# Kernel optimization log

Hardware: AMD Instinct MI355X
Metric: run time of the kernel (lower is better)

The kernel has to match this reference:

```python
import jax, jax.numpy as jnp
import numpy as np

INPUT_DIM = 24
HIDDEN = 128
NUM_LAYERS = 3
OUTPUT_DIM = 1


def _lstm_layer(x, Wih, Whh, bih, bhh):
    """Single LSTM layer, PyTorch gate order (i, f, g, o). x: [B,T,D] -> [B,T,H]."""
    B = x.shape[0]
    H = Whh.shape[1]
    # Precompute input projections for all timesteps at once: [B,T,4H]
    xg = jnp.einsum('btd,gd->btg', x, Wih) + bih
    xg = jnp.swapaxes(xg, 0, 1)  # [T,B,4H]
    h0 = jnp.zeros((B, H), x.dtype)
    c0 = jnp.zeros((B, H), x.dtype)

    def step(carry, xt):
        h, c = carry
        gates = xt + h @ Whh.T + bhh  # [B,4H]
        i, f, g, o = jnp.split(gates, 4, axis=-1)
        i = jax.nn.sigmoid(i)
        f = jax.nn.sigmoid(f)
        g = jnp.tanh(g)
        o = jax.nn.sigmoid(o)
        c = f * c + i * g
        h = o * jnp.tanh(c)
        return (h, c), h

    _, hs = jax.lax.scan(step, (h0, c0), xg)  # hs: [T,B,H]
    return jnp.swapaxes(hs, 0, 1)  # [B,T,H]


def setup_inputs() -> dict:
    key = jax.random.key(0)
    ks = jax.random.split(key, 16)
    B, T = 2048, 256
    s = 0.05
    inp = {
        'x': jax.random.normal(ks[0], (B, T, INPUT_DIM), dtype=jnp.float32),
    }
    dims_in = [INPUT_DIM, HIDDEN, HIDDEN]
    for l in range(NUM_LAYERS):
        inp[f'Wih{l}'] = jax.random.normal(ks[1 + 4 * l], (4 * HIDDEN, dims_in[l]), dtype=jnp.float32) * s
        inp[f'Whh{l}'] = jax.random.normal(ks[2 + 4 * l], (4 * HIDDEN, HIDDEN), dtype=jnp.float32) * s
        inp[f'bih{l}'] = jax.random.normal(ks[3 + 4 * l], (4 * HIDDEN,), dtype=jnp.float32) * s
        inp[f'bhh{l}'] = jax.random.normal(ks[4 + 4 * l], (4 * HIDDEN,), dtype=jnp.float32) * s
    inp['Wfc'] = jax.random.normal(ks[13], (OUTPUT_DIM, HIDDEN), dtype=jnp.float32) * s
    inp['bfc'] = jax.random.normal(ks[14], (OUTPUT_DIM,), dtype=jnp.float32) * s
    return inp


def reference(x, Wih0, Whh0, bih0, bhh0, Wih1, Whh1, bih1, bhh1,
              Wih2, Whh2, bih2, bhh2, Wfc, bfc):
    # 3 stacked LSTM layers (dropout inactive in eval mode), zero initial state.
    h = _lstm_layer(x, Wih0, Whh0, bih0, bhh0)
    h = _lstm_layer(h, Wih1, Whh1, bih1, bhh1)
    h = _lstm_layer(h, Wih2, Whh2, bih2, bhh2)
    # Linear projection of the final timestep: [B,1]
    return h[:, -1, :] @ Wfc.T + bfc
```

## Files before the change

### kernel.cpp

```cpp
#include <hip/hip_runtime.h>

#define T_STEPS 256
#define BATCH   2048
#define HID     128
#define ROWS    8

typedef short short8  __attribute__((ext_vector_type(8)));
typedef short short4v __attribute__((ext_vector_type(4)));
typedef float float4v __attribute__((ext_vector_type(4)));

template<bool B> struct BoolC { static constexpr bool value = B; };

__device__ __forceinline__ unsigned short f2bf(float f) {
    unsigned int u = __builtin_bit_cast(unsigned int, f);
    u += 0x7fffu + ((u >> 16) & 1u);
    return (unsigned short)(u >> 16);
}
__device__ __forceinline__ float bf2f(unsigned short b) {
    unsigned int u = ((unsigned int)b) << 16;
    return __builtin_bit_cast(float, u);
}

#if __has_builtin(__builtin_amdgcn_exp2f)
#define EXP2F(x) __builtin_amdgcn_exp2f(x)
#else
#define EXP2F(x) exp2f(x)
#endif
__device__ __forceinline__ float sigf(float x) {
    return __builtin_amdgcn_rcpf(1.0f + EXP2F(x * -1.442695041f));
}
__device__ __forceinline__ float tanh_fast(float x) {
    return 2.0f * __builtin_amdgcn_rcpf(1.0f + EXP2F(x * -2.885390082f)) - 1.0f;
}

__device__ __forceinline__ void block_sync_lds() {
    asm volatile("s_waitcnt lgkmcnt(0)" ::: "memory");
    __builtin_amdgcn_s_barrier();
    __builtin_amdgcn_sched_barrier(0);
}

__device__ __forceinline__ int lposH(int row, int off) {
    return row * 256 + (off ^ ((row & 7) << 4));
}
__device__ __forceinline__ int lposX(int row, int off) {
    return row * 256 + (off ^ ((row & 7) << 4));
}
__device__ __forceinline__ int lposX0(int row, int off) {
    return row * 64 + (off ^ ((row & 3) << 4));
}

__device__ __forceinline__ short8 load_w8(const float* __restrict__ p) {
    float4v a = *reinterpret_cast<const float4v*>(p);
    float4v b = *reinterpret_cast<const float4v*>(p + 4);
    short8 r;
    r[0] = (short)f2bf(a[0]); r[1] = (short)f2bf(a[1]);
    r[2] = (short)f2bf(a[2]); r[3] = (short)f2bf(a[3]);
    r[4] = (short)f2bf(b[0]); r[5] = (short)f2bf(b[1]);
    r[6] = (short)f2bf(b[2]); r[7] = (short)f2bf(b[3]);
    return r;
}

template<bool IS_L0, bool WRITE_H, bool FINAL>
__global__ __launch_bounds__(512, 2)
void lstm_layer(const float* __restrict__ x0,
                const float* __restrict__ Wih,
                const float* __restrict__ Whh,
                const float* __restrict__ bih,
                const float* __restrict__ bhh,
                unsigned short* __restrict__ hbuf,
                const float* __restrict__ Wfc,
                const float* __restrict__ bfc,
                float* __restrict__ out)
{
    constexpr int XKS = IS_L0 ? 1 : 4;
    constexpr int XRB = IS_L0 ? 64 : 256;
    constexpr int HB  = ROWS * 256;
    constexpr int XB  = 16 * XRB;
    constexpr int LDS_TOT = 2 * HB + 2 * XB;
    __shared__ __attribute__((aligned(16))) unsigned char a_lds[LDS_TOT];
    const int XS0 = 2 * HB, XS1 = 2 * HB + XB;

    const int tid  = threadIdx.x;
    const int lane = tid & 63;
    const int wv   = tid >> 6;
    const int b0   = blockIdx.x * ROWS;

    const int t16   = lane & 15;
    const int kgrp8 = (lane >> 4) * 8;
    const int jcol  = 16 * wv + t16;
    const int row0  = ((lane >> 4) & 1) * 4 + ((lane >> 5) & 1) * 2;

    const int g2   = t16 >> 2;
    const int hrow = ((g2 & 1) << 2) | ((g2 >> 1) << 1) | (t16 & 1);
    int aoffH[4];
    #pragma unroll
    for (int ks = 0; ks < 4; ++ks)
        aoffH[ks] = lposH(hrow, ks * 64 + kgrp8 * 2);
    int aoffX[XKS];
    #pragma unroll
    for (int s = 0; s < XKS; ++s)
        aoffX[s] = IS_L0 ? lposX0(t16, kgrp8 * 2)
                         : lposX(t16, s * 64 + kgrp8 * 2);

    const int hwoff0 = lposH(row0,     2 * jcol);
    const int hwoff1 = lposH(row0 + 1, 2 * jcol);

    const int srow4 = tid >> 6, scol4 = tid & 63;
    const int hroff4 = lposH(srow4, scol4 * 4);
    const size_t sgoff4 = (size_t)(b0 + srow4) * HID + scol4 * 2;

    const int sar = tid >> 5, sc8 = tid & 31;
    const int sb  = (sar & 1) | (((sar >> 3) & 1) << 1) | (((sar >> 2) & 1) << 2);
    const int ss  = (sar >> 1) & 1;
    const int xwoff = lposX(sar, sc8 * 8);
    const size_t xgrow = (size_t)(b0 + sb) * HID + sc8 * 4;
    const bool xvalid = tid < 384;
    const int ar0 = xvalid ? tid / 24 : 0, xc = xvalid ? tid % 24 : 0;
    const int xb_ = (ar0 & 1) | (((ar0 >> 3) & 1) << 1) | (((ar0 >> 2) & 1) << 2);
    const int xs  = (ar0 >> 1) & 1;
    const int xw0off = lposX0(ar0, xc * 2);
    const size_t x0row = (size_t)(b0 + xb_) * (T_STEPS * 24) + xc;

    short8 wfh[4][4], wfx[4][XKS];
    float  bias[4];
    #pragma unroll
    for (int q = 0; q < 4; ++q) {
        const int n = 128 * q + jcol;
        bias[q] = bih[n] + bhh[n];
        #pragma unroll
        for (int ks = 0; ks < 4; ++ks)
            wfh[q][ks] = load_w8(Whh + n * 128 + ks * 32 + kgrp8);
        if (IS_L0) {
            if (kgrp8 < 24) wfx[q][0] = load_w8(Wih + n * 24 + kgrp8);
            else            { short8 z = {0,0,0,0,0,0,0,0}; wfx[q][0] = z; }
        } else {
            #pragma unroll
            for (int s = 0; s < 4; ++s)
                wfx[q][s] = load_w8(Wih + n * 128 + s * 32 + kgrp8);
        }
    }

    {
        short8 z = {0,0,0,0,0,0,0,0};
        for (int i = tid * 16; i < LDS_TOT; i += 512 * 16)
            *reinterpret_cast<short8*>(&a_lds[i]) = z;
    }
    __syncthreads();

    short4v xpre = {0, 0, 0, 0};
    float   xpref = 0.f;
    if (!IS_L0) {
        short4v v = *reinterpret_cast<const short4v*>(
            &hbuf[(size_t)(0 + ss) * (BATCH * HID) + xgrow]);
        *reinterpret_cast<short4v*>(&a_lds[XS0 + xwoff]) = v;
        xpre = *reinterpret_cast<const short4v*>(
            &hbuf[(size_t)(2 + ss) * (BATCH * HID) + xgrow]);
    } else if (xvalid) {
        float v = x0[x0row + (size_t)(0 + xs) * 24];
        *reinterpret_cast<unsigned short*>(&a_lds[XS0 + xw0off]) = f2bf(v);
        xpref = x0[x0row + (size_t)(2 + xs) * 24];
    }
    __syncthreads();

    float4v xacc[4];
    #pragma unroll
    for (int q = 0; q < 4; ++q)
        xacc[q] = float4v{bias[q], bias[q], bias[q], bias[q]};
    {
        short8 xa[XKS];
        #pragma unroll
        for (int s = 0; s < XKS; ++s)
            xa[s] = *reinterpret_cast<const short8*>(&a_lds[XS0 + aoffX[s]]);
        #pragma unroll
        for (int s = 0; s < XKS; ++s)
            #pragma unroll
            for (int q = 0; q < 4; ++q)
                xacc[q] = __builtin_amdgcn_mfma_f32_16x16x32_bf16(xa[s], wfx[q][s], xacc[q], 0, 0, 0);
    }

    float creg[2] = {0.f, 0.f};

    auto do_step = [&](int t, auto ODDC) {
        constexpr bool ODD = decltype(ODDC)::value;
        const int rb = ODD ? HB : 0;
        const int wb = ODD ? 0 : HB;
        if (WRITE_H && t > 0) {
            unsigned int hv = *reinterpret_cast<const unsigned int*>(&a_lds[rb + hroff4]);
            *reinterpret_cast<unsigned int*>(
                &hbuf[(size_t)(t - 1) * (BATCH * HID) + sgoff4]) = hv;
        }
        if constexpr (!ODD) {
            const int xsb = ((((t >> 1) & 1) ^ 1) ? XS1 : XS0);
            if (!IS_L0) {
                if (t + 2 + ss < T_STEPS)
                    *reinterpret_cast<short4v*>(&a_lds[xsb + xwoff]) = xpre;
            } else if (xvalid && (t + 2 + xs < T_STEPS))
                *reinterpret_cast<unsigned short*>(&a_lds[xsb + xw0off]) = f2bf(xpref);
        } else {
            if (!IS_L0) {
                if (t + 3 + ss < T_STEPS)
                    xpre = *reinterpret_cast<const short4v*>(
                        &hbuf[(size_t)(t + 3 + ss) * (BATCH * HID) + xgrow]);
            } else if (xvalid && (t + 3 + xs < T_STEPS))
                xpref = x0[x0row + (size_t)(t + 3 + xs) * 24];
        }
        float4v acc[4];
        #pragma unroll
        for (int q = 0; q < 4; ++q) {
            const float a = ODD ? xacc[q][2] : xacc[q][0];
            const float b = ODD ? xacc[q][3] : xacc[q][1];
            acc[q] = float4v{a, b, a, b};
        }
        short8 hva[4];
        #pragma unroll
        for (int ks = 0; ks < 4; ++ks)
            hva[ks] = *reinterpret_cast<const short8*>(&a_lds[rb + aoffH[ks]]);
        __builtin_amdgcn_s_setprio(1);
        #pragma unroll
        for (int ks = 0; ks < 4; ++ks)
            #pragma unroll
            for (int q = 0; q < 4; ++q)
                acc[q] = __builtin_amdgcn_mfma_f32_16x16x32_bf16(hva[ks], wfh[q][ks], acc[q], 0, 0, 0);
        if constexpr (ODD) {
            if (t + 1 < T_STEPS) {
                const int xrb_ = ((((t + 1) >> 1) & 1) ? XS1 : XS0);
                #pragma unroll
                for (int q = 0; q < 4; ++q)
                    xacc[q] = float4v{bias[q], bias[q], bias[q], bias[q]};
                short8 xa[XKS];
                #pragma unroll
                for (int s = 0; s < XKS; ++s)
                    xa[s] = *reinterpret_cast<const short8*>(&a_lds[xrb_ + aoffX[s]]);
                #pragma unroll
                for (int s = 0; s < XKS; ++s)
                    #pragma unroll
                    for (int q = 0; q < 4; ++q)
                        xacc[q] = __builtin_amdgcn_mfma_f32_16x16x32_bf16(xa[s], wfx[q][s], xacc[q], 0, 0, 0);
            }
        }
        __builtin_amdgcn_s_setprio(0);
        const float c0 = sigf(acc[1][0]) * creg[0] + sigf(acc[0][0]) * tanh_fast(acc[2][0]);
        const float c1 = sigf(acc[1][1]) * creg[1] + sigf(acc[0][1]) * tanh_fast(acc[2][1]);
        creg[0] = c0;  creg[1] = c1;
        const float h0 = sigf(acc[3][0]) * tanh_fast(c0);
        const float h1 = sigf(acc[3][1]) * tanh_fast(c1);
        unsigned int packed;
        asm("v_cvt_pk_bf16_f32 %0, %1, %2" : "=v"(packed) : "v"(h0), "v"(h1));
        *reinterpret_cast<unsigned short*>(&a_lds[wb + hwoff0]) =
            (unsigned short)(packed & 0xffffu);
        *reinterpret_cast<unsigned short*>(&a_lds[wb + hwoff1]) =
            (unsigned short)(packed >> 16);
        block_sync_lds();
    };

    for (int th = 0; th < T_STEPS / 2; ++th) {
        do_step(2 * th,     BoolC<false>{});
        do_step(2 * th + 1, BoolC<true>{});
    }
    if (WRITE_H) {
        unsigned int hv = *reinterpret_cast<const unsigned int*>(&a_lds[hroff4]);
        *reinterpret_cast<unsigned int*>(
            &hbuf[(size_t)(T_STEPS - 1) * (BATCH * HID) + sgoff4]) = hv;
    }
    if (FINAL && tid < 128) {
        const int r = tid >> 4, seg = tid & 15;
        float s = 0.f;
        #pragma unroll
        for (int k = 0; k < 8; ++k) {
            const int j = seg * 8 + k;
            s += bf2f(*reinterpret_cast<const unsigned short*>(&a_lds[lposH(r, 2 * j)]))
                 * Wfc[j];
        }
        #pragma unroll
        for (int off = 8; off >= 1; off >>= 1) s += __shfl_xor(s, off);
        if (seg == 0) out[b0 + r] = s + bfc[0];
    }
}

extern "C" void kernel_launch(void* const* d_in, const int* in_sizes, int n_in,
                              void* d_out, int out_size, void* d_ws, size_t ws_size,
                              hipStream_t stream) {
    (void)in_sizes; (void)n_in; (void)out_size; (void)ws_size;
    const float* x    = (const float*)d_in[0];
    const float* Wih0 = (const float*)d_in[1];
    const float* Whh0 = (const float*)d_in[2];
    const float* bih0 = (const float*)d_in[3];
    const float* bhh0 = (const float*)d_in[4];
    const float* Wih1 = (const float*)d_in[5];
    const float* Whh1 = (const float*)d_in[6];
    const float* bih1 = (const float*)d_in[7];
    const float* bhh1 = (const float*)d_in[8];
    const float* Wih2 = (const float*)d_in[9];
    const float* Whh2 = (const float*)d_in[10];
    const float* bih2 = (const float*)d_in[11];
    const float* bhh2 = (const float*)d_in[12];
    const float* Wfc  = (const float*)d_in[13];
    const float* bfc  = (const float*)d_in[14];
    float* out = (float*)d_out;
    unsigned short* hbuf = (unsigned short*)d_ws;

    dim3 grid(BATCH / ROWS), block(512);
    lstm_layer<true,  true,  false><<<grid, block, 0, stream>>>(x,       Wih0, Whh0, bih0, bhh0, hbuf, nullptr, nullptr, nullptr);
    lstm_layer<false, true,  false><<<grid, block, 0, stream>>>(nullptr, Wih1, Whh1, bih1, bhh1, hbuf, nullptr, nullptr, nullptr);
    lstm_layer<false, false, true ><<<grid, block, 0, stream>>>(nullptr, Wih2, Whh2, bih2, bhh2, hbuf, Wfc,     bfc,     out);
}
```

Before: 569.0 us.

## Fuse three LSTM layer kernels into one persistent kernel and hoist step loads

Replaces the three per-layer launches with a single kernel that runs all three layers in sequence inside each block. This works because each block only ever consumes its own batch rows from the hidden-state buffer. LDS is sized to the largest layer and reused across phases. Within each timestep, the h and x operand LDS reads are issued first and the next-step input-projection MFMAs run before the recurrent MFMAs, to hide LDS latency. The aim is to remove inter-launch gaps and per-layer tail effects. The cost is a longer kernel with possible register-pressure changes.

```diff
diff --git a/kernel.cpp b/kernel.cpp
--- a/kernel.cpp
+++ b/kernel.cpp
@@ -60,30 +60,30 @@
     return r;
 }
 
+#define LDS_BYTES 12288
+
 template<bool IS_L0, bool WRITE_H, bool FINAL>
-__global__ __launch_bounds__(512, 2)
-void lstm_layer(const float* __restrict__ x0,
-                const float* __restrict__ Wih,
-                const float* __restrict__ Whh,
-                const float* __restrict__ bih,
-                const float* __restrict__ bhh,
-                unsigned short* __restrict__ hbuf,
-                const float* __restrict__ Wfc,
-                const float* __restrict__ bfc,
-                float* __restrict__ out)
+__device__ __forceinline__ void lstm_phase(
+    unsigned char* a_lds,
+    const float* __restrict__ x0,
+    const float* __restrict__ Wih,
+    const float* __restrict__ Whh,
+    const float* __restrict__ bih,
+    const float* __restrict__ bhh,
+    unsigned short* __restrict__ hbuf,
+    const float* __restrict__ Wfc,
+    const float* __restrict__ bfc,
+    float* __restrict__ out,
+    const int tid, const int b0)
 {
     constexpr int XKS = IS_L0 ? 1 : 4;
     constexpr int XRB = IS_L0 ? 64 : 256;
     constexpr int HB  = ROWS * 256;
     constexpr int XB  = 16 * XRB;
-    constexpr int LDS_TOT = 2 * HB + 2 * XB;
-    __shared__ __attribute__((aligned(16))) unsigned char a_lds[LDS_TOT];
     const int XS0 = 2 * HB, XS1 = 2 * HB + XB;
 
-    const int tid  = threadIdx.x;
     const int lane = tid & 63;
     const int wv   = tid >> 6;
-    const int b0   = blockIdx.x * ROWS;
 
     const int t16   = lane & 15;
     const int kgrp8 = (lane >> 4) * 8;
@@ -142,8 +142,12 @@
 
     {
         short8 z = {0,0,0,0,0,0,0,0};
-        for (int i = tid * 16; i < LDS_TOT; i += 512 * 16)
-            *reinterpret_cast<short8*>(&a_lds[i]) = z;
+        #pragma unroll
+        for (int i = 0; i < 2; ++i) {
+            const int a = tid * 16 + i * 8192;
+            if (a < LDS_BYTES)
+                *reinterpret_cast<short8*>(&a_lds[a]) = z;
+        }
     }
     __syncthreads();
 
@@ -184,6 +188,25 @@
         constexpr bool ODD = decltype(ODDC)::value;
         const int rb = ODD ? HB : 0;
         const int wb = ODD ? 0 : HB;
+        short8 hva[4];
+        #pragma unroll
+        for (int ks = 0; ks < 4; ++ks)
+            hva[ks] = *reinterpret_cast<const short8*>(&a_lds[rb + aoffH[ks]]);
+        short8 xa[XKS];
+        const bool do_x = ODD && (t + 1 < T_STEPS);
+        if (do_x) {
+            const int xrb_ = ((((t + 1) >> 1) & 1) ? XS1 : XS0);
+            #pragma unroll
+            for (int s = 0; s < XKS; ++s)
+                xa[s] = *reinterpret_cast<const short8*>(&a_lds[xrb_ + aoffX[s]]);
+        }
+        float4v acc[4];
+        #pragma unroll
+        for (int q = 0; q < 4; ++q) {
+            const float a = ODD ? xacc[q][2] : xacc[q][0];
+            const float b = ODD ? xacc[q][3] : xacc[q][1];
+            acc[q] = float4v{a, b, a, b};
+        }
         if (WRITE_H && t > 0) {
             unsigned int hv = *reinterpret_cast<const unsigned int*>(&a_lds[rb + hroff4]);
             *reinterpret_cast<unsigned int*>(
@@ -204,40 +227,22 @@
             } else if (xvalid && (t + 3 + xs < T_STEPS))
                 xpref = x0[x0row + (size_t)(t + 3 + xs) * 24];
         }
-        float4v acc[4];
-        #pragma unroll
-        for (int q = 0; q < 4; ++q) {
-            const float a = ODD ? xacc[q][2] : xacc[q][0];
-            const float b = ODD ? xacc[q][3] : xacc[q][1];
-            acc[q] = float4v{a, b, a, b};
-        }
-        short8 hva[4];
-        #pragma unroll
-        for (int ks = 0; ks < 4; ++ks)
-            hva[ks] = *reinterpret_cast<const short8*>(&a_lds[rb + aoffH[ks]]);
         __builtin_amdgcn_s_setprio(1);
+        if (do_x) {
+            #pragma unroll
+            for (int q = 0; q < 4; ++q)
+                xacc[q] = float4v{bias[q], bias[q], bias[q], bias[q]};
+            #pragma unroll
+            for (int s = 0; s < XKS; ++s)
+                #pragma unroll
+                for (int q = 0; q < 4; ++q)
+                    xacc[q] = __builtin_amdgcn_mfma_f32_16x16x32_bf16(xa[s], wfx[q][s], xacc[q], 0, 0, 0);
+        }
         #pragma unroll
         for (int ks = 0; ks < 4; ++ks)
             #pragma unroll
             for (int q = 0; q < 4; ++q)
                 acc[q] = __builtin_amdgcn_mfma_f32_16x16x32_bf16(hva[ks], wfh[q][ks], acc[q], 0, 0, 0);
-        if constexpr (ODD) {
-            if (t + 1 < T_STEPS) {
-                const int xrb_ = ((((t + 1) >> 1) & 1) ? XS1 : XS0);
-                #pragma unroll
-                for (int q = 0; q < 4; ++q)
-                    xacc[q] = float4v{bias[q], bias[q], bias[q], bias[q]};
-                short8 xa[XKS];
-                #pragma unroll
-                for (int s = 0; s < XKS; ++s)
-                    xa[s] = *reinterpret_cast<const short8*>(&a_lds[xrb_ + aoffX[s]]);
-                #pragma unroll
-                for (int s = 0; s < XKS; ++s)
-                    #pragma unroll
-                    for (int q = 0; q < 4; ++q)
-                        xacc[q] = __builtin_amdgcn_mfma_f32_16x16x32_bf16(xa[s], wfx[q][s], xacc[q], 0, 0, 0);
-            }
-        }
         __builtin_amdgcn_s_setprio(0);
         const float c0 = sigf(acc[1][0]) * creg[0] + sigf(acc[0][0]) * tanh_fast(acc[2][0]);
         const float c1 = sigf(acc[1][1]) * creg[1] + sigf(acc[0][1]) * tanh_fast(acc[2][1]);
@@ -275,6 +280,31 @@
         for (int off = 8; off >= 1; off >>= 1) s += __shfl_xor(s, off);
         if (seg == 0) out[b0 + r] = s + bfc[0];
     }
+}
+
+__global__ __launch_bounds__(512, 2)
+void lstm3(const float* __restrict__ x0,
+           const float* __restrict__ Wih0, const float* __restrict__ Whh0,
+           const float* __restrict__ bih0, const float* __restrict__ bhh0,
+           const float* __restrict__ Wih1, const float* __restrict__ Whh1,
+           const float* __restrict__ bih1, const float* __restrict__ bhh1,
+           const float* __restrict__ Wih2, const float* __restrict__ Whh2,
+           const float* __restrict__ bih2, const float* __restrict__ bhh2,
+           const float* __restrict__ Wfc,  const float* __restrict__ bfc,
+           unsigned short* __restrict__ hbuf, float* __restrict__ out)
+{
+    __shared__ __attribute__((aligned(16))) unsigned char a_lds[LDS_BYTES];
+    const int tid = threadIdx.x;
+    const int b0  = blockIdx.x * ROWS;
+
+    lstm_phase<true,  true,  false>(a_lds, x0, Wih0, Whh0, bih0, bhh0, hbuf,
+                                    nullptr, nullptr, nullptr, tid, b0);
+    __syncthreads();
+    lstm_phase<false, true,  false>(a_lds, nullptr, Wih1, Whh1, bih1, bhh1, hbuf,
+                                    nullptr, nullptr, nullptr, tid, b0);
+    __syncthreads();
+    lstm_phase<false, false, true >(a_lds, nullptr, Wih2, Whh2, bih2, bhh2, hbuf,
+                                    Wfc, bfc, out, tid, b0);
 }
 
 extern "C" void kernel_launch(void* const* d_in, const int* in_sizes, int n_in,
@@ -300,7 +330,8 @@
     unsigned short* hbuf = (unsigned short*)d_ws;
 
     dim3 grid(BATCH / ROWS), block(512);
-    lstm_layer<true,  true,  false><<<grid, block, 0, stream>>>(x,       Wih0, Whh0, bih0, bhh0, hbuf, nullptr, nullptr, nullptr);
-    lstm_layer<false, true,  false><<<grid, block, 0, stream>>>(nullptr, Wih1, Whh1, bih1, bhh1, hbuf, nullptr, nullptr, nullptr);
-    lstm_layer<false, false, true ><<<grid, block, 0, stream>>>(nullptr, Wih2, Whh2, bih2, bhh2, hbuf, Wfc,     bfc,     out);
-}
+    lstm3<<<grid, block, 0, stream>>>(x, Wih0, Whh0, bih0, bhh0,
+                                      Wih1, Whh1, bih1, bhh1,
+                                      Wih2, Whh2, bih2, bhh2,
+                                      Wfc, bfc, hbuf, out);
+}
```

New measurement: 592.5 us. +4.1%, slower.
